# Performance work log

Hardware: AMD Instinct MI355X
Metric: run time of the kernel (lower is better)

Reference implementation:

```python
import jax, jax.numpy as jnp
import numpy as np

DIM = 512
NUM_HEADS = 8
HEAD_DIM = DIM // NUM_HEADS
REL_POS_BINS = 961
B, N = 64, 256


def setup_inputs() -> dict:
    key = jax.random.key(0)
    ks = jax.random.split(key, 7)
    x = jax.random.normal(ks[0], (B, N, DIM), dtype=jnp.float32)
    rel_pos_index = jax.random.randint(ks[1], (N, N), 0, REL_POS_BINS)
    s = 1.0 / np.sqrt(DIM)
    qkv_w = jax.random.normal(ks[2], (3 * DIM, DIM), dtype=jnp.float32) * s
    qkv_b = jax.random.normal(ks[3], (3 * DIM,), dtype=jnp.float32) * 0.02
    proj_w = jax.random.normal(ks[4], (DIM, DIM), dtype=jnp.float32) * s
    proj_b = jax.random.normal(ks[5], (DIM,), dtype=jnp.float32) * 0.02
    rel_pos_bias = jax.random.normal(ks[6], (NUM_HEADS, REL_POS_BINS), dtype=jnp.float32) * 0.02
    return {"x": x, "rel_pos_index": rel_pos_index, "qkv_w": qkv_w,
            "qkv_b": qkv_b, "proj_w": proj_w, "proj_b": proj_b,
            "rel_pos_bias": rel_pos_bias}


def reference(x, rel_pos_index, qkv_w, qkv_b, proj_w, proj_b, rel_pos_bias):
    Bn, Nn, C = x.shape
    H, D = NUM_HEADS, HEAD_DIM
    qkv = x @ qkv_w.T + qkv_b                      # (B,N,3C)
    qkv = qkv.reshape(Bn, Nn, 3, H, D).transpose(2, 0, 3, 1, 4)  # (3,B,H,N,D)
    q, k, v = qkv[0], qkv[1], qkv[2]
    scale = 1.0 / jnp.sqrt(jnp.asarray(D, dtype=x.dtype))
    scores = jnp.einsum('bhnd,bhmd->bhnm', q, k) * scale          # (B,H,N,N)
    bias = rel_pos_bias[:, rel_pos_index]                          # (H,N,N) gather
    scores = scores + bias[None]
    attn = jax.nn.softmax(scores, axis=-1)
    out = jnp.einsum('bhnm,bhmd->bhnd', attn, v)                   # (B,H,N,D)
    out = out.transpose(0, 2, 1, 3).reshape(Bn, Nn, C)
    return out @ proj_w.T + proj_b
```

## Files before the change

### kernel.cpp

```cpp
#include <hip/hip_runtime.h>
#include <stdint.h>

#define DIM 512
#define NHEADS 8
#define HDIM 64
#define NBINS 961
#define BATCH 64
#define SEQ 256
#define NTOK (BATCH*SEQ)
#define BHND (BATCH*NHEADS*SEQ*HDIM)

using bf16x8 = __attribute__((ext_vector_type(8))) short;
using f32x4  = __attribute__((ext_vector_type(4))) float;

__device__ __forceinline__ unsigned short f2bf(float f) {
  unsigned u = __float_as_uint(f);
  u += 0x7FFF + ((u >> 16) & 1);
  return (unsigned short)(u >> 16);
}

__device__ __forceinline__ void async16(const void* g, void* lds) {
  __builtin_amdgcn_global_load_lds(
      (const __attribute__((address_space(1))) unsigned int*)g,
      (__attribute__((address_space(3))) unsigned int*)lds,
      16, 0, 0);
}


__global__ void cast_kernel(const float* __restrict__ in,
                            unsigned short* __restrict__ out, int n4) {
  int i = blockIdx.x * 256 + threadIdx.x;
  if (i >= n4) return;
  float4 f = reinterpret_cast<const float4*>(in)[i];
  ushort4 o;
  o.x = f2bf(f.x); o.y = f2bf(f.y); o.z = f2bf(f.z); o.w = f2bf(f.w);
  reinterpret_cast<ushort4*>(out)[i] = o;
}

__global__ void bias_kernel(const int* __restrict__ idx,
                            const float* __restrict__ rpb,
                            float* __restrict__ bf) {
  int i = blockIdx.x * 256 + threadIdx.x;
  if (i >= NHEADS * SEQ * SEQ) return;
  int h = i >> 16;
  int r = i & 65535;
  int n = r >> 8, m = r & 255;
  bf[(size_t)h * 65536 + n * 256 + (m & 15) * 16 + (m >> 4)] = rpb[h * NBINS + idx[r]];
}


__device__ __forceinline__ void stage_half(const unsigned short* __restrict__ X,
                                           int row0, int kk, char* dst, int t) {
#pragma unroll
  for (int i = 0; i < 2; ++i) {
    int q = i * 512 + t;
    int r = q >> 3, s = q & 7;
    const unsigned short* src = X + (size_t)(row0 + r) * 512 + kk + ((s ^ (r & 7)) << 3);
    async16(src, dst + (size_t)(i * 512 + ((t >> 6) << 6)) * 16);
  }
}

template<int NBW, int EPI>
__global__ __launch_bounds__(512) void gemm8p(
    const unsigned short* __restrict__ A,
    const unsigned short* __restrict__ Bw,
    const float* __restrict__ bias,
    void* __restrict__ outp, int nbn, int cpx) {
  extern __shared__ char gsm[];
  constexpr int BN   = NBW * 64;
  constexpr int BUF  = 32768 + NBW * 8192;
  const int t = threadIdx.x;
  const int lane = t & 63, l15 = lane & 15, lg = lane >> 4;
  const int wv = t >> 6, wm = wv & 1, wn = wv >> 1;
  const int bid = blockIdx.x;
  const int nid = (bid & 7) * cpx + (bid >> 3);
  const int m0 = (nid / nbn) * 256, n0 = (nid % nbn) * BN;

  f32x4 acc[8][NBW];
  const f32x4 fz = {0.f, 0.f, 0.f, 0.f};
#pragma unroll
  for (int a = 0; a < 8; ++a)
#pragma unroll
    for (int b = 0; b < NBW; ++b) acc[a][b] = fz;

  stage_half(A,  m0,       0, gsm,          t);
  stage_half(A,  m0 + 128, 0, gsm + 16384,  t);
  stage_half(Bw, n0,       0, gsm + 32768,  t);
  if (NBW == 4) stage_half(Bw, n0 + 128, 0, gsm + 49152, t);

  int cur = 0;
#pragma unroll 1
  for (int T = 0; T < 8; ++T) {
    char* Ab  = gsm + cur * BUF;
    char* Bb  = Ab + 32768;
    char* nxt = gsm + (cur ^ 1) * BUF;

    __builtin_amdgcn_s_barrier();
    if (T < 7) {
      stage_half(A, m0,       (T + 1) * 64, nxt,         t);
      stage_half(A, m0 + 128, (T + 1) * 64, nxt + 16384, t);
      asm volatile("s_waitcnt vmcnt(4)" ::: "memory");
    } else {
      asm volatile("s_waitcnt vmcnt(0)" ::: "memory");
    }
    __builtin_amdgcn_sched_barrier(0);

#pragma unroll
    for (int ph = 0; ph < 4; ++ph) {
      const int kh = ph >> 1, mh = ph & 1;
      if (ph == 1 && T < 7) stage_half(Bw, n0, (T + 1) * 64, nxt + 32768, t);
      if (NBW == 4 && ph == 2 && T < 7) stage_half(Bw, n0 + 128, (T + 1) * 64, nxt + 49152, t);

      const int sw = ((kh * 4 + lg) ^ (l15 & 7)) * 16;
      bf16x8 av[4], bv[NBW];
#pragma unroll
      for (int mi = 0; mi < 4; ++mi)
        av[mi] = *(const bf16x8*)(Ab + wm * 16384 + (mh * 64 + mi * 16 + l15) * 128 + sw);
#pragma unroll
      for (int ni = 0; ni < NBW; ++ni) {
        int rb = wn * (NBW * 16) + ni * 16 + l15;
        bv[ni] = *(const bf16x8*)(Bb + (rb >> 7) * 16384 + (rb & 127) * 128 + sw);
      }
      asm volatile("s_waitcnt lgkmcnt(0)" ::: "memory");
      __builtin_amdgcn_sched_barrier(0);
      __builtin_amdgcn_s_setprio(1);
#pragma unroll
      for (int mi = 0; mi < 4; ++mi)
#pragma unroll
        for (int ni = 0; ni < NBW; ++ni)
          acc[mh * 4 + mi][ni] =
              __builtin_amdgcn_mfma_f32_16x16x32_bf16(av[mi], bv[ni], acc[mh * 4 + mi][ni], 0, 0, 0);
      __builtin_amdgcn_s_setprio(0);
      __builtin_amdgcn_sched_barrier(0);
    }
    cur ^= 1;
  }

#pragma unroll
  for (int MI = 0; MI < 8; ++MI)
#pragma unroll
    for (int ni = 0; ni < NBW; ++ni)
#pragma unroll
      for (int r = 0; r < 4; ++r) {
        int row = m0 + wm * 128 + MI * 16 + lg * 4 + r;
        int col = n0 + wn * (NBW * 16) + ni * 16 + l15;
        float v = acc[MI][ni][r] + bias[col];
        if (EPI == 0) {
          int which = col >> 9, hd = col & 511;
          int b = row >> 8, n = row & 255;
          ((unsigned short*)outp)[(size_t)which * BHND +
              (((size_t)(b * NHEADS + (hd >> 6)) * SEQ + n) * HDIM) + (hd & 63)] = f2bf(v);
        } else {
          ((float*)outp)[(size_t)row * 512 + col] = v;
        }
      }
}


__global__ __launch_bounds__(256) void attn_kernel(
    const unsigned short* __restrict__ qb,
    const unsigned short* __restrict__ kb,
    const unsigned short* __restrict__ vb,
    const float* __restrict__ biasf,
    unsigned short* __restrict__ aout) {
  extern __shared__ char smem[];
  char* k_s = smem;
  char* v_s = smem + 32768;
  const int t = threadIdx.x, lane = t & 63, w = t >> 6;
  const int l15 = lane & 15, lg = lane >> 4;
  char* P_s = smem + w * 2048;
  const int nid = (blockIdx.x & 7) * 256 + (blockIdx.x >> 3);
  const int bh = nid >> 2, quarter = nid & 3;
  const int h = bh & 7;
  const int b = bh >> 3;
  const int row0 = quarter * 64 + w * 16;
  const size_t base = (size_t)bh * (SEQ * HDIM);

#pragma unroll
  for (int i = 0; i < 8; ++i) {
    int c = i * 256 + t;
    int row = c >> 3, sl = c & 7;
    bf16x8 val = *(const bf16x8*)(kb + base + (size_t)c * 8);
    *(bf16x8*)(k_s + row * 128 + ((sl * 16) ^ ((row & 7) << 4))) = val;
  }
#pragma unroll
  for (int i = 0; i < 8; ++i) {
    int c = i * 256 + t;
    int key = c >> 3, d0 = (c & 7) * 8;
    bf16x8 val = *(const bf16x8*)(vb + base + (size_t)c * 8);
#pragma unroll
    for (int j = 0; j < 8; ++j) {
      int d = d0 + j;
      int term = (((d & 7) ^ ((d >> 3) & 7)) << 4);
      *(short*)(v_s + d * 512 + ((key * 2) ^ term)) = val[j];
    }
  }
  bf16x8 qa[2];
#pragma unroll
  for (int ks = 0; ks < 2; ++ks)
    qa[ks] = *(const bf16x8*)(qb + base + (size_t)(row0 + l15) * 64 + ks * 32 + lg * 8);
  __syncthreads();

  f32x4 accs[16];
  const f32x4 fz = {0.f, 0.f, 0.f, 0.f};
#pragma unroll
  for (int c = 0; c < 16; ++c) accs[c] = fz;
  __builtin_amdgcn_s_setprio(1);
#pragma unroll
  for (int cf = 0; cf < 16; ++cf) {
    int key = cf * 16 + l15;
#pragma unroll
    for (int ks = 0; ks < 2; ++ks) {
      bf16x8 kf = *(const bf16x8*)(k_s + key * 128 + ((lg * 16 + ks * 64) ^ ((key & 7) << 4)));
      accs[cf] = __builtin_amdgcn_mfma_f32_16x16x32_bf16(qa[ks], kf, accs[cf], 0, 0, 0);
    }
  }
  __builtin_amdgcn_s_setprio(0);

  const float* bh_ptr = biasf + (size_t)h * 65536;
#pragma unroll
  for (int r = 0; r < 4; ++r) {
    int n = row0 + lg * 4 + r;
    const f32x4* bp = (const f32x4*)(bh_ptr + n * 256 + l15 * 16);
    f32x4 b0 = bp[0], b1 = bp[1], b2 = bp[2], b3 = bp[3];
#pragma unroll
    for (int cf = 0; cf < 16; ++cf) {
      float bb = (cf < 4) ? b0[cf] : (cf < 8) ? b1[cf - 4] : (cf < 12) ? b2[cf - 8] : b3[cf - 12];
      accs[cf][r] = accs[cf][r] * 0.125f + bb;
    }
  }

  float pinv[4];
#pragma unroll
  for (int r = 0; r < 4; ++r) {
    float m = -1e30f;
#pragma unroll
    for (int cf = 0; cf < 16; ++cf) m = fmaxf(m, accs[cf][r]);
#pragma unroll
    for (int off = 1; off < 16; off <<= 1) m = fmaxf(m, __shfl_xor(m, off, 64));
    float s = 0.f;
#pragma unroll
    for (int cf = 0; cf < 16; ++cf) {
      float p = __expf(accs[cf][r] - m);
      accs[cf][r] = p;
      s += p;
    }
#pragma unroll
    for (int off = 1; off < 16; off <<= 1) s += __shfl_xor(s, off, 64);
    pinv[r] = 1.0f / s;
  }

  __syncthreads();

  f32x4 acco[4];
#pragma unroll
  for (int c2 = 0; c2 < 4; ++c2) acco[c2] = fz;

  for (int ch = 0; ch < 4; ++ch) {
#pragma unroll
    for (int cl = 0; cl < 4; ++cl)
#pragma unroll
      for (int r = 0; r < 4; ++r) {
        int rowl = lg * 4 + r;
        int ml = cl * 16 + l15;
        float p = accs[ch * 4 + cl][r] * pinv[r];
        *(short*)(P_s + rowl * 128 + ((ml * 2) ^ ((rowl & 7) << 4))) = (short)f2bf(p);
      }
#pragma unroll
    for (int ks = 0; ks < 2; ++ks) {
      bf16x8 pa = *(const bf16x8*)(P_s + l15 * 128 + ((lg * 16 + ks * 64) ^ ((l15 & 7) << 4)));
      int keyb = (ch * 64 + ks * 32 + lg * 8) * 2;
      __builtin_amdgcn_s_setprio(1);
#pragma unroll
      for (int df = 0; df < 4; ++df) {
        int d = df * 16 + l15;
        int term = (((d & 7) ^ ((d >> 3) & 7)) << 4);
        bf16x8 vf = *(const bf16x8*)(v_s + d * 512 + (keyb ^ term));
        acco[df] = __builtin_amdgcn_mfma_f32_16x16x32_bf16(pa, vf, acco[df], 0, 0, 0);
      }
      __builtin_amdgcn_s_setprio(0);
    }
  }

#pragma unroll
  for (int df = 0; df < 4; ++df)
#pragma unroll
    for (int r = 0; r < 4; ++r) {
      int n = row0 + lg * 4 + r;
      int d = df * 16 + l15;
      aout[((size_t)(b * SEQ + n)) * DIM + h * HDIM + d] = f2bf(acco[df][r]);
    }
}


extern "C" void kernel_launch(void* const* d_in, const int* in_sizes, int n_in,
                              void* d_out, int out_size, void* d_ws, size_t ws_size,
                              hipStream_t stream) {
  const float* x      = (const float*)d_in[0];
  const int*   rpi    = (const int*)d_in[1];
  const float* qkv_w  = (const float*)d_in[2];
  const float* qkv_b  = (const float*)d_in[3];
  const float* proj_w = (const float*)d_in[4];
  const float* proj_b = (const float*)d_in[5];
  const float* rpb    = (const float*)d_in[6];

  char* ws = (char*)d_ws;
  unsigned short* xb    = (unsigned short*)ws;
  unsigned short* wqkv  = (unsigned short*)(ws + 16777216);
  unsigned short* wproj = (unsigned short*)(ws + 18350080);
  float*          biasf = (float*)         (ws + 18874368);
  unsigned short* qkvb  = (unsigned short*)(ws + 20971520);
  unsigned short* aoutb = (unsigned short*)(ws + 71303168);

  cast_kernel<<<8192, 256, 0, stream>>>(x, xb, 2097152);
  cast_kernel<<<768, 256, 0, stream>>>(qkv_w, wqkv, 196608);
  cast_kernel<<<256, 256, 0, stream>>>(proj_w, wproj, 65536);
  bias_kernel<<<2048, 256, 0, stream>>>(rpi, rpb, biasf);

  gemm8p<4, 0><<<384, 512, 131072, stream>>>(xb, wqkv, qkv_b, (void*)qkvb, 6, 48);

  attn_kernel<<<2048, 256, 65536, stream>>>(qkvb, qkvb + BHND, qkvb + 2 * (size_t)BHND,
                                            biasf, aoutb);

  gemm8p<2, 1><<<256, 512, 98304, stream>>>(aoutb, wproj, proj_b, d_out, 4, 32);
}
```

Before: 108.6 us.

## Restructure GEMM staging into K-halves and read attention K from global memory

```diff
diff --git a/kernel.cpp b/kernel.cpp
--- a/kernel.cpp
+++ b/kernel.cpp
@@ -24,6 +24,12 @@
       (const __attribute__((address_space(1))) unsigned int*)g,
       (__attribute__((address_space(3))) unsigned int*)lds,
       16, 0, 0);
+}
+
+template<int N> __device__ __forceinline__ void waitv() {
+  if constexpr (N == 0) asm volatile("s_waitcnt vmcnt(0)" ::: "memory");
+  else if constexpr (N == 3) asm volatile("s_waitcnt vmcnt(3)" ::: "memory");
+  else if constexpr (N == 4) asm volatile("s_waitcnt vmcnt(4)" ::: "memory");
 }
 
 
@@ -49,89 +55,96 @@
 }
 
 
-__device__ __forceinline__ void stage_half(const unsigned short* __restrict__ X,
-                                           int row0, int kk, char* dst, int t) {
-#pragma unroll
-  for (int i = 0; i < 2; ++i) {
+template<int NLOAD>
+__device__ __forceinline__ void stage_kh(const unsigned short* __restrict__ X,
+                                         int row0, int kk, char* dst, int t) {
+#pragma unroll
+  for (int i = 0; i < NLOAD; ++i) {
     int q = i * 512 + t;
-    int r = q >> 3, s = q & 7;
-    const unsigned short* src = X + (size_t)(row0 + r) * 512 + kk + ((s ^ (r & 7)) << 3);
+    int r = q >> 2, c = q & 3;
+    const unsigned short* src = X + (size_t)(row0 + r) * 512 + kk + ((c ^ ((r >> 1) & 3)) << 3);
     async16(src, dst + (size_t)(i * 512 + ((t >> 6) << 6)) * 16);
   }
 }
 
-template<int NBW, int EPI>
-__global__ __launch_bounds__(512) void gemm8p(
+template<int NB, int EPI>
+__global__ __launch_bounds__(512, 2) void gemm_k2(
     const unsigned short* __restrict__ A,
     const unsigned short* __restrict__ Bw,
     const float* __restrict__ bias,
     void* __restrict__ outp, int nbn, int cpx) {
   extern __shared__ char gsm[];
-  constexpr int BN   = NBW * 64;
-  constexpr int BUF  = 32768 + NBW * 8192;
+  constexpr int ASZ = 16384;
+  constexpr int BSZ = NB * 8192;
+  constexpr int BUF = 2 * ASZ + 2 * BSZ;
+  constexpr int NI  = 2 * NB;
+  constexpr int VW  = 2 + NB;
   const int t = threadIdx.x;
   const int lane = t & 63, l15 = lane & 15, lg = lane >> 4;
   const int wv = t >> 6, wm = wv & 1, wn = wv >> 1;
   const int bid = blockIdx.x;
   const int nid = (bid & 7) * cpx + (bid >> 3);
-  const int m0 = (nid / nbn) * 256, n0 = (nid % nbn) * BN;
-
-  f32x4 acc[8][NBW];
+  const int m0 = (nid / nbn) * 256, n0 = (nid % nbn) * (NB * 128);
+
+  f32x4 acc[8][NI];
   const f32x4 fz = {0.f, 0.f, 0.f, 0.f};
 #pragma unroll
   for (int a = 0; a < 8; ++a)
 #pragma unroll
-    for (int b = 0; b < NBW; ++b) acc[a][b] = fz;
-
-  stage_half(A,  m0,       0, gsm,          t);
-  stage_half(A,  m0 + 128, 0, gsm + 16384,  t);
-  stage_half(Bw, n0,       0, gsm + 32768,  t);
-  if (NBW == 4) stage_half(Bw, n0 + 128, 0, gsm + 49152, t);
+    for (int b = 0; b < NI; ++b) acc[a][b] = fz;
+
+  stage_kh<2>(A,  m0, 0,  gsm, t);
+  stage_kh<NB>(Bw, n0, 0,  gsm + 2 * ASZ, t);
+  stage_kh<2>(A,  m0, 32, gsm + ASZ, t);
+  stage_kh<NB>(Bw, n0, 32, gsm + 2 * ASZ + BSZ, t);
+  waitv<VW>();
+  __builtin_amdgcn_s_barrier();
 
   int cur = 0;
 #pragma unroll 1
   for (int T = 0; T < 8; ++T) {
-    char* Ab  = gsm + cur * BUF;
-    char* Bb  = Ab + 32768;
-    char* nxt = gsm + (cur ^ 1) * BUF;
-
-    __builtin_amdgcn_s_barrier();
-    if (T < 7) {
-      stage_half(A, m0,       (T + 1) * 64, nxt,         t);
-      stage_half(A, m0 + 128, (T + 1) * 64, nxt + 16384, t);
-      asm volatile("s_waitcnt vmcnt(4)" ::: "memory");
-    } else {
-      asm volatile("s_waitcnt vmcnt(0)" ::: "memory");
-    }
-    __builtin_amdgcn_sched_barrier(0);
-
+    char* base = gsm + cur * BUF;
+    char* nxt  = gsm + (cur ^ 1) * BUF;
+    const int kn = (T + 1) * 64;
+
+    bf16x8 av[4], bv[NI];
 #pragma unroll
     for (int ph = 0; ph < 4; ++ph) {
       const int kh = ph >> 1, mh = ph & 1;
-      if (ph == 1 && T < 7) stage_half(Bw, n0, (T + 1) * 64, nxt + 32768, t);
-      if (NBW == 4 && ph == 2 && T < 7) stage_half(Bw, n0 + 128, (T + 1) * 64, nxt + 49152, t);
-
-      const int sw = ((kh * 4 + lg) ^ (l15 & 7)) * 16;
-      bf16x8 av[4], bv[NBW];
-#pragma unroll
-      for (int mi = 0; mi < 4; ++mi)
-        av[mi] = *(const bf16x8*)(Ab + wm * 16384 + (mh * 64 + mi * 16 + l15) * 128 + sw);
-#pragma unroll
-      for (int ni = 0; ni < NBW; ++ni) {
-        int rb = wn * (NBW * 16) + ni * 16 + l15;
-        bv[ni] = *(const bf16x8*)(Bb + (rb >> 7) * 16384 + (rb & 127) * 128 + sw);
-      }
+      char* Ah = base + kh * ASZ;
+      char* Bh = base + 2 * ASZ + kh * BSZ;
+#pragma unroll
+      for (int mi = 0; mi < 4; ++mi) {
+        int ra = wm * 128 + mh * 64 + mi * 16 + l15;
+        av[mi] = *(const bf16x8*)(Ah + ra * 64 + ((lg ^ ((ra >> 1) & 3)) * 16));
+      }
+      if (mh == 0) {
+#pragma unroll
+        for (int ni = 0; ni < NI; ++ni) {
+          int rb = wn * (NB * 32) + ni * 16 + l15;
+          bv[ni] = *(const bf16x8*)(Bh + rb * 64 + ((lg ^ ((rb >> 1) & 3)) * 16));
+        }
+      }
+      if (T < 7) {
+        if (ph == 0)      stage_kh<2>(A,  m0, kn,      nxt, t);
+        else if (ph == 1) stage_kh<NB>(Bw, n0, kn,      nxt + 2 * ASZ, t);
+        else if (ph == 2) stage_kh<2>(A,  m0, kn + 32, nxt + ASZ, t);
+        else              stage_kh<NB>(Bw, n0, kn + 32, nxt + 2 * ASZ + BSZ, t);
+      }
+      if (ph == 1) { if (T < 7) waitv<VW>(); else waitv<0>(); }
+      if (ph == 3 && T < 7) waitv<VW>();
+      __builtin_amdgcn_s_barrier();
       asm volatile("s_waitcnt lgkmcnt(0)" ::: "memory");
       __builtin_amdgcn_sched_barrier(0);
       __builtin_amdgcn_s_setprio(1);
 #pragma unroll
       for (int mi = 0; mi < 4; ++mi)
 #pragma unroll
-        for (int ni = 0; ni < NBW; ++ni)
+        for (int ni = 0; ni < NI; ++ni)
           acc[mh * 4 + mi][ni] =
               __builtin_amdgcn_mfma_f32_16x16x32_bf16(av[mi], bv[ni], acc[mh * 4 + mi][ni], 0, 0, 0);
       __builtin_amdgcn_s_setprio(0);
-      __builtin_amdgcn_sched_barrier(0);
+      __builtin_amdgcn_s_barrier();
     }
     cur ^= 1;
   }
@@ -139,11 +152,11 @@
 #pragma unroll
   for (int MI = 0; MI < 8; ++MI)
 #pragma unroll
-    for (int ni = 0; ni < NBW; ++ni)
+    for (int ni = 0; ni < NI; ++ni)
 #pragma unroll
       for (int r = 0; r < 4; ++r) {
         int row = m0 + wm * 128 + MI * 16 + lg * 4 + r;
-        int col = n0 + wn * (NBW * 16) + ni * 16 + l15;
+        int col = n0 + wn * (NB * 32) + ni * 16 + l15;
         float v = acc[MI][ni][r] + bias[col];
         if (EPI == 0) {
           int which = col >> 9, hd = col & 511;
@@ -157,18 +170,17 @@
 }
 
 
-__global__ __launch_bounds__(256) void attn_kernel(
+__global__ __launch_bounds__(256, 4) void attn_kernel(
     const unsigned short* __restrict__ qb,
     const unsigned short* __restrict__ kb,
     const unsigned short* __restrict__ vb,
     const float* __restrict__ biasf,
     unsigned short* __restrict__ aout) {
   extern __shared__ char smem[];
-  char* k_s = smem;
-  char* v_s = smem + 32768;
+  char* v_s = smem;
   const int t = threadIdx.x, lane = t & 63, w = t >> 6;
   const int l15 = lane & 15, lg = lane >> 4;
-  char* P_s = smem + w * 2048;
+  char* P_s = smem + 32768 + w * 2048;
   const int nid = (blockIdx.x & 7) * 256 + (blockIdx.x >> 3);
   const int bh = nid >> 2, quarter = nid & 3;
   const int h = bh & 7;
@@ -179,13 +191,6 @@
 #pragma unroll
   for (int i = 0; i < 8; ++i) {
     int c = i * 256 + t;
-    int row = c >> 3, sl = c & 7;
-    bf16x8 val = *(const bf16x8*)(kb + base + (size_t)c * 8);
-    *(bf16x8*)(k_s + row * 128 + ((sl * 16) ^ ((row & 7) << 4))) = val;
-  }
-#pragma unroll
-  for (int i = 0; i < 8; ++i) {
-    int c = i * 256 + t;
     int key = c >> 3, d0 = (c & 7) * 8;
     bf16x8 val = *(const bf16x8*)(vb + base + (size_t)c * 8);
 #pragma unroll
@@ -199,23 +204,21 @@
 #pragma unroll
   for (int ks = 0; ks < 2; ++ks)
     qa[ks] = *(const bf16x8*)(qb + base + (size_t)(row0 + l15) * 64 + ks * 32 + lg * 8);
-  __syncthreads();
-
+
+  const unsigned short* kbase = kb + base;
   f32x4 accs[16];
   const f32x4 fz = {0.f, 0.f, 0.f, 0.f};
 #pragma unroll
   for (int c = 0; c < 16; ++c) accs[c] = fz;
-  __builtin_amdgcn_s_setprio(1);
 #pragma unroll
   for (int cf = 0; cf < 16; ++cf) {
     int key = cf * 16 + l15;
 #pragma unroll
     for (int ks = 0; ks < 2; ++ks) {
-      bf16x8 kf = *(const bf16x8*)(k_s + key * 128 + ((lg * 16 + ks * 64) ^ ((key & 7) << 4)));
+      bf16x8 kf = *(const bf16x8*)(kbase + (size_t)key * 64 + ks * 32 + lg * 8);
       accs[cf] = __builtin_amdgcn_mfma_f32_16x16x32_bf16(qa[ks], kf, accs[cf], 0, 0, 0);
     }
   }
-  __builtin_amdgcn_s_setprio(0);
 
   const float* bh_ptr = biasf + (size_t)h * 65536;
 #pragma unroll
@@ -263,12 +266,14 @@
       for (int r = 0; r < 4; ++r) {
         int rowl = lg * 4 + r;
         int ml = cl * 16 + l15;
+        int pterm = (((rowl & 7) ^ ((rowl >> 2) & 2)) << 4);
         float p = accs[ch * 4 + cl][r] * pinv[r];
-        *(short*)(P_s + rowl * 128 + ((ml * 2) ^ ((rowl & 7) << 4))) = (short)f2bf(p);
+        *(short*)(P_s + rowl * 128 + ((ml * 2) ^ pterm)) = (short)f2bf(p);
       }
 #pragma unroll
     for (int ks = 0; ks < 2; ++ks) {
-      bf16x8 pa = *(const bf16x8*)(P_s + l15 * 128 + ((lg * 16 + ks * 64) ^ ((l15 & 7) << 4)));
+      int rterm = (((l15 & 7) ^ ((l15 >> 2) & 2)) << 4);
+      bf16x8 pa = *(const bf16x8*)(P_s + l15 * 128 + ((lg * 16 + ks * 64) ^ rterm));
       int keyb = (ch * 64 + ks * 32 + lg * 8) * 2;
       __builtin_amdgcn_s_setprio(1);
 #pragma unroll
@@ -317,10 +322,10 @@
   cast_kernel<<<256, 256, 0, stream>>>(proj_w, wproj, 65536);
   bias_kernel<<<2048, 256, 0, stream>>>(rpi, rpb, biasf);
 
-  gemm8p<4, 0><<<384, 512, 131072, stream>>>(xb, wqkv, qkv_b, (void*)qkvb, 6, 48);
-
-  attn_kernel<<<2048, 256, 65536, stream>>>(qkvb, qkvb + BHND, qkvb + 2 * (size_t)BHND,
+  gemm_k2<2, 0><<<384, 512, 131072, stream>>>(xb, wqkv, qkv_b, (void*)qkvb, 6, 48);
+
+  attn_kernel<<<2048, 256, 40960, stream>>>(qkvb, qkvb + BHND, qkvb + 2 * (size_t)BHND,
                                             biasf, aoutb);
 
-  gemm8p<2, 1><<<256, 512, 98304, stream>>>(aoutb, wproj, proj_b, d_out, 4, 32);
-}
+  gemm_k2<1, 1><<<256, 512, 98304, stream>>>(aoutb, wproj, proj_b, d_out, 4, 32);
+}
```

New measurement: 126.7 us. +16.7%, slower.
